# Optimization experiments

Measured on AMD Instinct MI355X. Metric: run time of the kernel, lower is better.

The kernel has to match this reference:

```python
import jax, jax.numpy as jnp
import numpy as np

VOCAB = 50257
EMB = 1024
HID = 1024
B, T = 8, 256


def setup_inputs() -> dict:
    key = jax.random.key(0)
    ks = jax.random.split(key, 6)
    s = 0.05  # small init scale for numerical sanity
    return {
        "x": jax.random.randint(ks[0], (B, T), 0, VOCAB, dtype=jnp.int64) if jax.config.jax_enable_x64 else jax.random.randint(ks[0], (B, T), 0, VOCAB, dtype=jnp.int32),
        "emb_W": jax.random.normal(ks[1], (VOCAB, EMB), dtype=jnp.float32) * s,
        "W_ih": jax.random.normal(ks[2], (4 * HID, EMB), dtype=jnp.float32) * s,
        "W_hh": jax.random.normal(ks[3], (4 * HID, HID), dtype=jnp.float32) * s,
        "b_ih": jax.random.normal(ks[4], (4 * HID,), dtype=jnp.float32) * s,
        "b_hh": jax.random.normal(ks[5], (4 * HID,), dtype=jnp.float32) * s,
        "dec_b": jnp.zeros((VOCAB,), dtype=jnp.float32),
    }


def _lstm(emb, W_ih, W_hh, b_ih, b_hh):
    # emb: [B, T, E]. Precompute input projections for all timesteps (one big GEMM).
    x_proj = jnp.einsum("bte,ge->btg", emb, W_ih) + (b_ih + b_hh)  # [B, T, 4H]
    h0 = jnp.zeros((emb.shape[0], HID), emb.dtype)
    c0 = jnp.zeros((emb.shape[0], HID), emb.dtype)

    def step(carry, xt):  # xt: [B, 4H]
        h, c = carry
        g = xt + h @ W_hh.T  # [B, 4H]
        i, f, gg, o = jnp.split(g, 4, axis=-1)  # PyTorch gate order i,f,g,o
        i = jax.nn.sigmoid(i)
        f = jax.nn.sigmoid(f)
        gg = jnp.tanh(gg)
        o = jax.nn.sigmoid(o)
        c_new = f * c + i * gg
        h_new = o * jnp.tanh(c_new)
        return (h_new, c_new), h_new

    (hT, cT), hs = jax.lax.scan(step, (h0, c0), jnp.swapaxes(x_proj, 0, 1))
    out = jnp.swapaxes(hs, 0, 1)  # [B, T, H], batch_first
    return out, (hT[None], cT[None])  # num_layers=1 leading dim


def reference(x, emb_W, W_ih, W_hh, b_ih, b_hh, dec_b):
    emb = emb_W[x]                                   # [B, T, E]
    out, hidden = _lstm(emb, W_ih, W_hh, b_ih, b_hh)  # [B, T, H]
    logits = jnp.einsum("bth,vh->btv", out, emb_W) + dec_b  # tied decoder
    logits = logits.reshape(-1, VOCAB)
    return jax.nn.log_softmax(logits, axis=1), hidden
```

## Files before the change

kernel.cpp:

```cpp
#include <hip/hip_runtime.h>

typedef float f32x4 __attribute__((ext_vector_type(4)));
typedef __bf16 bf16x8 __attribute__((ext_vector_type(8)));
typedef unsigned int u32x4 __attribute__((ext_vector_type(4)));
typedef unsigned short u16;
typedef unsigned int u32;

#define VOCAB 50257
#define KDIM 1024
#define MROWS 2048
#define TSEQ 256
#define NBLK 64
#define NHELP 192
#define NTILE 393
#define NT (NTILE * 2)
#define LOGN ((size_t)MROWS * VOCAB)

__device__ __forceinline__ u16 f2bf(float f) {
    u32 u = __builtin_bit_cast(u32, f);
    u = (u + 0x7FFFu + ((u >> 16) & 1u)) >> 16;
    return (u16)u;
}

__device__ __forceinline__ float sigm(float x) { return 1.0f / (1.0f + __expf(-x)); }

__device__ __forceinline__ u32 min4u(u32x4 v) {
    u32 a = v.x < v.y ? v.x : v.y;
    u32 b = v.z < v.w ? v.z : v.w;
    return a < b ? a : b;
}

__device__ __forceinline__ ushort4 cvt4(float4 v) {
    ushort4 o;
    o.x = f2bf(v.x); o.y = f2bf(v.y); o.z = f2bf(v.z); o.w = f2bf(v.w);
    return o;
}


__global__ __launch_bounds__(256)
void prep_all(const float4* __restrict__ Wih, ushort4* __restrict__ Wih_bf,
              const float4* __restrict__ Whh, ushort4* __restrict__ Whh_bf,
              const int* __restrict__ x, const float* __restrict__ embW,
              ushort4* __restrict__ emb_bf, u32* __restrict__ hseq,
              const float* __restrict__ bih, const float* __restrict__ bhh,
              float* __restrict__ bsum)
{
    const int bid = blockIdx.x, tid = threadIdx.x;
    if (bid < 4096) {
        long i = (long)bid * 256 + tid;
        Wih_bf[i] = cvt4(Wih[i]);
    } else if (bid < 8192) {
        long i = (long)(bid - 4096) * 256 + tid;
        Whh_bf[i] = cvt4(Whh[i]);
    } else if (bid < 10240) {
        int m = bid - 8192;
        int row = x[m];
        float4 v = ((const float4*)(embW + (size_t)row * KDIM))[tid];
        emb_bf[(size_t)m * 256 + tid] = cvt4(v);
    } else if (bid < 14352) {
        int i = (bid - 10240) * 256 + tid;
        hseq[i] = (i < 4096) ? 0x00010001u : 0u;
    } else {
        int i = (bid - 14352) * 256 + tid;
        if (i < 4096) bsum[i] = bih[i] + bhh[i];
    }
}


#define BM 128
#define BN 128
#define BK 64

__device__ __forceinline__ void gl_lds16(const u16* g, const u16* l) {
    __builtin_amdgcn_global_load_lds(
        (const __attribute__((address_space(1))) u32*)g,
        (__attribute__((address_space(3))) u32*)l, 16, 0, 0);
}

__global__ __launch_bounds__(256, 2)
void gemm_bt(const u16* __restrict__ A, const u16* __restrict__ Bm,
             const float* __restrict__ bias, float* __restrict__ C,
             int N, int Nb, int K, int ldc)
{
    __shared__ __align__(16) u16 As[BM * BK];
    __shared__ __align__(16) u16 Bs[BN * BK];
    const int tid  = threadIdx.x;
    const int lane = tid & 63;
    const int wid  = tid >> 6;

    const int gx  = gridDim.x;
    const int nwg = gx * gridDim.y;
    const int lin = blockIdx.y * gx + blockIdx.x;
    const int qq = nwg >> 3, rr = nwg & 7;
    const int xcd = lin & 7, idx = lin >> 3;
    const int neu = (xcd < rr) ? (xcd * (qq + 1) + idx)
                               : (rr * (qq + 1) + (xcd - rr) * qq + idx);
    const int bm = neu % gx;
    const int bn = neu / gx;

    const int wr = wid >> 1, wc = wid & 1;

    const u16* gA[4]; const u16* gB[4];
    const u16* ldsA[4]; const u16* ldsB[4];
#pragma unroll
    for (int r = 0; r < 4; ++r) {
        int L = r * 256 + tid;
        int row = L >> 3, ps = L & 7;
        int ls = ps ^ (row & 7);
        gA[r] = A + (size_t)(bm * BM + row) * K + ls * 8;
        int brow = bn * BN + row; brow = brow < Nb ? brow : Nb - 1;
        gB[r] = Bm + (size_t)brow * K + ls * 8;
        ldsA[r] = As + (r * 256 + wid * 64) * 8;
        ldsB[r] = Bs + (r * 256 + wid * 64) * 8;
    }

    const int lrow = lane & 15, ksl = lane >> 4;
    int aoff[4][2], boff[4][2];
#pragma unroll
    for (int i = 0; i < 4; ++i)
#pragma unroll
        for (int ks = 0; ks < 2; ++ks) {
            int ar = wr * 64 + i * 16 + lrow;
            aoff[i][ks] = ar * BK + (((ks * 4 + ksl) ^ (ar & 7)) * 8);
            int br = wc * 64 + i * 16 + lrow;
            boff[i][ks] = br * BK + (((ks * 4 + ksl) ^ (br & 7)) * 8);
        }

    f32x4 acc[4][4] = {};
    for (int kt = 0; kt < K; kt += BK) {
#pragma unroll
        for (int r = 0; r < 4; ++r) gl_lds16(gA[r] + kt, ldsA[r]);
#pragma unroll
        for (int r = 0; r < 4; ++r) gl_lds16(gB[r] + kt, ldsB[r]);
        __syncthreads();
        bf16x8 af[4][2], bfb[4][2];
#pragma unroll
        for (int i = 0; i < 4; ++i)
#pragma unroll
            for (int ks = 0; ks < 2; ++ks) {
                af[i][ks]  = *(const bf16x8*)(As + aoff[i][ks]);
                bfb[i][ks] = *(const bf16x8*)(Bs + boff[i][ks]);
            }
#pragma unroll
        for (int ks = 0; ks < 2; ++ks)
#pragma unroll
            for (int mi = 0; mi < 4; ++mi)
#pragma unroll
                for (int ni = 0; ni < 4; ++ni)
                    acc[mi][ni] = __builtin_amdgcn_mfma_f32_16x16x32_bf16(
                        af[mi][ks], bfb[ni][ks], acc[mi][ni], 0, 0, 0);
        __syncthreads();
    }

    const int crl = lane >> 4, ccl = lane & 15;
    const int row0 = bm * BM + wr * 64, col0 = bn * BN + wc * 64;
#pragma unroll
    for (int ni = 0; ni < 4; ++ni) {
        int col = col0 + ni * 16 + ccl;
        if (col < N) {
            float bv = bias[col];
#pragma unroll
            for (int mi = 0; mi < 4; ++mi) {
                int row = row0 + mi * 16 + crl * 4;
                float* cp = C + (size_t)row * ldc + col;
#pragma unroll
                for (int r = 0; r < 4; ++r)
                    cp[(size_t)r * ldc] = acc[mi][ni][r] + bv;
            }
        }
    }
}


__global__ __launch_bounds__(256, 3)
void gemm_dec(const u16* __restrict__ A, const u16* __restrict__ Bm,
              const float* __restrict__ bias, u16* __restrict__ Cb,
              float* __restrict__ pmax, float* __restrict__ psum)
{
    const int N = VOCAB, Nb = VOCAB, K = KDIM;
    __shared__ __align__(16) u16 As[BM * BK];
    __shared__ __align__(16) u16 Bs[BN * BK];
    const int tid  = threadIdx.x;
    const int lane = tid & 63;
    const int wid  = tid >> 6;

    const int gx  = gridDim.x;
    const int nwg = gx * gridDim.y;
    const int lin = blockIdx.y * gx + blockIdx.x;
    const int qq = nwg >> 3, rr = nwg & 7;
    const int xcd = lin & 7, idx = lin >> 3;
    const int neu = (xcd < rr) ? (xcd * (qq + 1) + idx)
                               : (rr * (qq + 1) + (xcd - rr) * qq + idx);
    const int bm = neu % gx;
    const int bn = neu / gx;

    const int wr = wid >> 1, wc = wid & 1;

    const u16* gA[4]; const u16* gB[4];
    const u16* ldsA[4]; const u16* ldsB[4];
#pragma unroll
    for (int r = 0; r < 4; ++r) {
        int L = r * 256 + tid;
        int row = L >> 3, ps = L & 7;
        int ls = ps ^ (row & 7);
        gA[r] = A + (size_t)(bm * BM + row) * K + ls * 8;
        int brow = bn * BN + row; brow = brow < Nb ? brow : Nb - 1;
        gB[r] = Bm + (size_t)brow * K + ls * 8;
        ldsA[r] = As + (r * 256 + wid * 64) * 8;
        ldsB[r] = Bs + (r * 256 + wid * 64) * 8;
    }

    const int lrow = lane & 15, ksl = lane >> 4;
    int aoff[4][2], boff[4][2];
#pragma unroll
    for (int i = 0; i < 4; ++i)
#pragma unroll
        for (int ks = 0; ks < 2; ++ks) {
            int ar = wr * 64 + i * 16 + lrow;
            aoff[i][ks] = ar * BK + (((ks * 4 + ksl) ^ (ar & 7)) * 8);
            int br = wc * 64 + i * 16 + lrow;
            boff[i][ks] = br * BK + (((ks * 4 + ksl) ^ (br & 7)) * 8);
        }

    f32x4 acc[4][4] = {};
    for (int kt = 0; kt < K; kt += BK) {
#pragma unroll
        for (int r = 0; r < 4; ++r) gl_lds16(gA[r] + kt, ldsA[r]);
#pragma unroll
        for (int r = 0; r < 4; ++r) gl_lds16(gB[r] + kt, ldsB[r]);
        __syncthreads();
        bf16x8 af[4][2], bfb[4][2];
#pragma unroll
        for (int i = 0; i < 4; ++i)
#pragma unroll
            for (int ks = 0; ks < 2; ++ks) {
                af[i][ks]  = *(const bf16x8*)(As + aoff[i][ks]);
                bfb[i][ks] = *(const bf16x8*)(Bs + boff[i][ks]);
            }
#pragma unroll
        for (int ks = 0; ks < 2; ++ks)
#pragma unroll
            for (int mi = 0; mi < 4; ++mi)
#pragma unroll
                for (int ni = 0; ni < 4; ++ni)
                    acc[mi][ni] = __builtin_amdgcn_mfma_f32_16x16x32_bf16(
                        af[mi][ks], bfb[ni][ks], acc[mi][ni], 0, 0, 0);
        __syncthreads();
    }

    const int crl = lane >> 4, ccl = lane & 15;
    const int row0 = bm * BM + wr * 64, col0 = bn * BN + wc * 64;
    float bve[4]; bool vld[4];
#pragma unroll
    for (int ni = 0; ni < 4; ++ni) {
        int col = col0 + ni * 16 + ccl;
        vld[ni] = col < N;
        bve[ni] = vld[ni] ? bias[col] : 0.f;
    }
#pragma unroll
    for (int ni = 0; ni < 4; ++ni) {
        if (vld[ni]) {
            int col = col0 + ni * 16 + ccl;
#pragma unroll
            for (int mi = 0; mi < 4; ++mi) {
                int row = row0 + mi * 16 + crl * 4;
                u16* cp = Cb + (size_t)row * (VOCAB * 2) + col;
#pragma unroll
                for (int r = 0; r < 4; ++r)
                    cp[(size_t)r * (VOCAB * 2)] = f2bf(acc[mi][ni][r] + bve[ni]);
            }
        }
    }
#pragma unroll
    for (int mi = 0; mi < 4; ++mi)
#pragma unroll
        for (int r = 0; r < 4; ++r) {
            int row = row0 + mi * 16 + crl * 4 + r;
            float v0 = vld[0] ? acc[mi][0][r] + bve[0] : -3.0e38f;
            float v1 = vld[1] ? acc[mi][1][r] + bve[1] : -3.0e38f;
            float v2 = vld[2] ? acc[mi][2][r] + bve[2] : -3.0e38f;
            float v3 = vld[3] ? acc[mi][3][r] + bve[3] : -3.0e38f;
            float rmax = fmaxf(fmaxf(v0, v1), fmaxf(v2, v3));
#pragma unroll
            for (int m2 = 1; m2 < 16; m2 <<= 1) rmax = fmaxf(rmax, __shfl_xor(rmax, m2));
            float rs = __expf(v0 - rmax) + __expf(v1 - rmax) +
                       __expf(v2 - rmax) + __expf(v3 - rmax);
#pragma unroll
            for (int m2 = 1; m2 < 16; m2 <<= 1) rs += __shfl_xor(rs, m2);
            if (ccl == 0) {
                pmax[(size_t)row * NT + bn * 2 + wc] = rmax;
                psum[(size_t)row * NT + bn * 2 + wc] = rs;
            }
        }
}


__global__ __launch_bounds__(256, 1)
void lstm_persist(const u16* __restrict__ Whh,
                  const float* __restrict__ xproj,
                  u16* __restrict__ hseq,
                  u16* __restrict__ hall,
                  float* __restrict__ outTail,
                  const float4* __restrict__ embW,
                  ushort4* __restrict__ embW_bf)
{
    const int tid = threadIdx.x;
    const int bid = blockIdx.x;

    if (bid >= NBLK) {
        long i = (long)(bid - NBLK) * 256 + tid;
        const long n4 = (long)VOCAB * KDIM / 4;
        const long stride = (long)NHELP * 256;
        for (; i < n4; i += stride) {
            float4 v = embW[i];
            embW_bf[i] = cvt4(v);
        }
        return;
    }

    const int lane = tid & 63;
    const int wq   = tid >> 6;
    const int lrow = lane & 15, ksl = lane >> 4;
    const int colbase = bid * 16;

    bf16x8 Bf[32];
    {
        const u16* bp = Whh + (size_t)(wq * 1024 + colbase + lrow) * KDIM + ksl * 8;
#pragma unroll
        for (int kk = 0; kk < 32; ++kk)
            asm volatile("global_load_dwordx4 %0, %1, off"
                         : "=v"(Bf[kk]) : "v"(bp + kk * 32));
        asm volatile("s_waitcnt vmcnt(0)" ::: "memory");
        __builtin_amdgcn_sched_barrier(0);
    }

    __shared__ float S[4][8][16];
    __shared__ __align__(16) u16 hstage[2][16384];

    for (int i = tid; i < 2 * 64 * 8; i += 256) {
        int buf = i >> 9, rem = i & 511;
        int j = rem >> 3, rowoff = rem & 7;
        u32x4 z = {0, 0, 0, 0};
        *(u32x4*)(&hstage[buf][j * 256 + 128 + rowoff * 16]) = z;
        *(u32x4*)(&hstage[buf][j * 256 + 128 + rowoff * 16 + 8]) = z;
    }

    const bool upd = tid < 128;
    const int b8 = tid >> 4, c16 = tid & 15;
    float creg = 0.f;
    float xp0 = 0.f, xp1 = 0.f, xp2 = 0.f, xp3 = 0.f;
    size_t xbase = 0;
    if (upd) {
        xbase = (size_t)b8 * TSEQ * 4096 + colbase + c16;
        xp0 = xproj[xbase];          xp1 = xproj[xbase + 1024];
        xp2 = xproj[xbase + 2048];   xp3 = xproj[xbase + 3072];
    }

    const int pj = tid >> 2, pr = (tid & 3) * 2;
    const int sw = (pj & 7) << 3;
    int widx[4];
#pragma unroll
    for (int k = 0; k < 4; ++k)
        widx[k] = pj * 256 + ((pr * 16 + k * 8) ^ sw);

    int aro[4];
#pragma unroll
    for (int i = 0; i < 4; ++i) {
        int swr = ((2 * i + (ksl >> 1)) & 7) << 3;
        aro[i] = (ksl >> 1) * 256 + ((lrow * 16 + (ksl & 1) * 8) ^ swr);
    }

    for (int t = 0; t < TSEQ; ++t) {
        const u32* src = (const u32*)hseq + (size_t)t * 4096 + pj * 64 + pr * 8;
        u32x4 P0, P1, P2, P3;
        for (;;) {
            asm volatile("global_load_dwordx4 %0, %1, off sc0 sc1" : "=v"(P0) : "v"(src));
            asm volatile("global_load_dwordx4 %0, %1, off sc0 sc1" : "=v"(P1) : "v"(src + 4));
            asm volatile("global_load_dwordx4 %0, %1, off sc0 sc1" : "=v"(P2) : "v"(src + 8));
            asm volatile("global_load_dwordx4 %0, %1, off sc0 sc1" : "=v"(P3) : "v"(src + 12));
            asm volatile("s_waitcnt vmcnt(0)" ::: "memory");
            __builtin_amdgcn_sched_barrier(0);
            u32 a = min4u(P0), b = min4u(P1), c = min4u(P2), d = min4u(P3);
            u32 mn = (a < b ? a : b); u32 mn2 = (c < d ? c : d);
            if ((mn < mn2 ? mn : mn2) != 0u) break;
        }
        {
            u16* hb2 = &hstage[t & 1][0];
            *(u32x4*)(hb2 + widx[0]) = P0;
            *(u32x4*)(hb2 + widx[1]) = P1;
            *(u32x4*)(hb2 + widx[2]) = P2;
            *(u32x4*)(hb2 + widx[3]) = P3;
        }
        __syncthreads();

        const u16* sb = &hstage[t & 1][0];
        f32x4 ac0 = {}, ac1 = {}, ac2 = {}, ac3 = {};
#pragma unroll
        for (int g = 0; g < 8; ++g) {
            bf16x8 a0 = *(const bf16x8*)(sb + g * 2048 + 0 * 512 + aro[0]);
            bf16x8 a1 = *(const bf16x8*)(sb + g * 2048 + 1 * 512 + aro[1]);
            bf16x8 a2 = *(const bf16x8*)(sb + g * 2048 + 2 * 512 + aro[2]);
            bf16x8 a3 = *(const bf16x8*)(sb + g * 2048 + 3 * 512 + aro[3]);
            ac0 = __builtin_amdgcn_mfma_f32_16x16x32_bf16(a0, Bf[g * 4 + 0], ac0, 0, 0, 0);
            ac1 = __builtin_amdgcn_mfma_f32_16x16x32_bf16(a1, Bf[g * 4 + 1], ac1, 0, 0, 0);
            ac2 = __builtin_amdgcn_mfma_f32_16x16x32_bf16(a2, Bf[g * 4 + 2], ac2, 0, 0, 0);
            ac3 = __builtin_amdgcn_mfma_f32_16x16x32_bf16(a3, Bf[g * 4 + 3], ac3, 0, 0, 0);
        }
        if (ksl < 2) {
#pragma unroll
            for (int r = 0; r < 4; ++r)
                S[wq][ksl * 4 + r][lrow] = ac0[r] + ac1[r] + ac2[r] + ac3[r];
        }
        __syncthreads();

        if (upd) {
            float gi = S[0][b8][c16] + xp0;
            float gf = S[1][b8][c16] + xp1;
            float gg = S[2][b8][c16] + xp2;
            float go = S[3][b8][c16] + xp3;
            float iv = sigm(gi), fv = sigm(gf), ov = sigm(go);
            float gv = tanhf(gg);
            creg = fv * creg + iv * gv;
            float hv = ov * tanhf(creg);
            u16 hbx = f2bf(hv) | 1;
            int w0 = (int)hbx;
            int w1 = __shfl_down(w0, 1);
            if (!(c16 & 1)) {
                u32 w = (u32)(u16)w0 | ((u32)(u16)w1 << 16);
                u32* dst = (u32*)hseq + (size_t)(t + 1) * 4096 + bid * 64 + b8 * 8 + (c16 >> 1);
                __hip_atomic_store(dst, w, __ATOMIC_RELAXED, __HIP_MEMORY_SCOPE_AGENT);
            }
            hall[((size_t)b8 * TSEQ + t) * KDIM + colbase + c16] = hbx;
            if (t == TSEQ - 1) {
                outTail[b8 * KDIM + colbase + c16] = hv;
                outTail[8192 + b8 * KDIM + colbase + c16] = creg;
            }
            int tn = (t + 1 < TSEQ) ? t + 1 : t;
            size_t xb = xbase + (size_t)tn * 4096;
            xp0 = xproj[xb];        xp1 = xproj[xb + 1024];
            xp2 = xproj[xb + 2048]; xp3 = xproj[xb + 3072];
        }
    }
}


__global__ __launch_bounds__(256)
void merge_final(const float* __restrict__ pmax, const float* __restrict__ psum,
                 float* __restrict__ out)
{
    const int m = blockIdx.x;
    const int tid = threadIdx.x;
    __shared__ float smx[4], ssm[4], slse;

    float mx = -3.0e38f, s = 0.f;
    for (int i = tid; i < NT; i += 256) {
        float pm = pmax[(size_t)m * NT + i];
        float ps = psum[(size_t)m * NT + i];
        if (pm > mx) { s *= __expf(mx - pm); mx = pm; }
        s += ps * __expf(pm - mx);
    }
#pragma unroll
    for (int off = 32; off > 0; off >>= 1) {
        float om = __shfl_xor(mx, off), os = __shfl_xor(s, off);
        float nm = fmaxf(mx, om);
        s = s * __expf(mx - nm) + os * __expf(om - nm);
        mx = nm;
    }
    if ((tid & 63) == 0) { smx[tid >> 6] = mx; ssm[tid >> 6] = s; }
    __syncthreads();
    if (tid == 0) {
        float M = fmaxf(fmaxf(smx[0], smx[1]), fmaxf(smx[2], smx[3]));
        float S4 = ssm[0] * __expf(smx[0] - M) + ssm[1] * __expf(smx[1] - M) +
                   ssm[2] * __expf(smx[2] - M) + ssm[3] * __expf(smx[3] - M);
        slse = M + __logf(S4);
    }
    __syncthreads();
    const float L = slse;

    const u32* srcw = (const u32*)out + (size_t)m * VOCAB;
    float* dst = out + (size_t)m * VOCAB;
    const int NCH = (VOCAB + 2047) / 2048;
    for (int c = NCH - 1; c >= 0; --c) {
        int e0 = c * 2048 + tid * 8;
        int w0i = e0 >> 1;
        u32 w0 = srcw[w0i], w1 = srcw[w0i + 1], w2 = srcw[w0i + 2], w3 = srcw[w0i + 3];
        __syncthreads();
        float f[8];
        f[0] = __builtin_bit_cast(float, (w0 & 0xFFFFu) << 16) - L;
        f[1] = __builtin_bit_cast(float, w0 & 0xFFFF0000u) - L;
        f[2] = __builtin_bit_cast(float, (w1 & 0xFFFFu) << 16) - L;
        f[3] = __builtin_bit_cast(float, w1 & 0xFFFF0000u) - L;
        f[4] = __builtin_bit_cast(float, (w2 & 0xFFFFu) << 16) - L;
        f[5] = __builtin_bit_cast(float, w2 & 0xFFFF0000u) - L;
        f[6] = __builtin_bit_cast(float, (w3 & 0xFFFFu) << 16) - L;
        f[7] = __builtin_bit_cast(float, w3 & 0xFFFF0000u) - L;
        if (e0 + 8 <= VOCAB) {
#pragma unroll
            for (int k = 0; k < 8; ++k) dst[e0 + k] = f[k];
        } else {
#pragma unroll
            for (int k = 0; k < 8; ++k) if (e0 + k < VOCAB) dst[e0 + k] = f[k];
        }
    }
}


extern "C" void kernel_launch(void* const* d_in, const int* in_sizes, int n_in,
                              void* d_out, int out_size, void* d_ws, size_t ws_size,
                              hipStream_t stream)
{
    const int*   x    = (const int*)d_in[0];
    const float* embW = (const float*)d_in[1];
    const float* Wih  = (const float*)d_in[2];
    const float* Whh  = (const float*)d_in[3];
    const float* bih  = (const float*)d_in[4];
    const float* bhh  = (const float*)d_in[5];
    const float* decb = (const float*)d_in[6];
    float* out = (float*)d_out;

    char* p = (char*)d_ws;
    auto carve = [&](size_t bytes) {
        char* q = p;
        p += (bytes + 255) & ~(size_t)255;
        return q;
    };
    u16*   embW_bf = (u16*)carve((size_t)VOCAB * KDIM * 2);
    u16*   Wih_bf  = (u16*)carve((size_t)4096 * KDIM * 2);
    u16*   Whh_bf  = (u16*)carve((size_t)4096 * KDIM * 2);
    u16*   emb_bf  = (u16*)carve((size_t)MROWS * KDIM * 2);
    float* xproj   = (float*)carve((size_t)MROWS * 4096 * 4);
    u16*   hall_bf = (u16*)carve((size_t)MROWS * KDIM * 2);
    u16*   hseq    = (u16*)carve((size_t)(TSEQ + 1) * 4096 * 4);
    float* pmax    = (float*)carve((size_t)MROWS * NT * 4);
    float* psum    = (float*)carve((size_t)MROWS * NT * 4);
    float* bsum    = (float*)carve((size_t)4096 * 4);

    prep_all<<<14368, 256, 0, stream>>>((const float4*)Wih, (ushort4*)Wih_bf,
                                        (const float4*)Whh, (ushort4*)Whh_bf,
                                        x, embW, (ushort4*)emb_bf,
                                        (u32*)hseq, bih, bhh, bsum);

    {
        dim3 g(MROWS / BM, 4096 / BN);
        gemm_bt<<<g, 256, 0, stream>>>(emb_bf, Wih_bf, bsum, xproj, 4096, 4096, KDIM, 4096);
    }

    lstm_persist<<<NBLK + NHELP, 256, 0, stream>>>(Whh_bf, xproj, hseq, hall_bf,
                                                   out + LOGN,
                                                   (const float4*)embW,
                                                   (ushort4*)embW_bf);

    {
        dim3 g(MROWS / BM, NTILE);
        gemm_dec<<<g, 256, 0, stream>>>(hall_bf, embW_bf, decb, (u16*)out, pmax, psum);
    }

    merge_final<<<MROWS, 256, 0, stream>>>(pmax, psum, out);
}
```

Before: 1.200 ms.

## Move embedding bf16 conversion from LSTM helper blocks into prep kernel

The tied-decoder weight conversion to bf16 previously ran in extra helper blocks launched alongside the persistent LSTM recurrence. It now runs as extra blocks of the prep kernel, so the LSTM launches only its 64 recurrence blocks. The aim is to stop the bandwidth-heavy conversion from contending with the latency-sensitive recurrence, at the cost of serializing the conversion before the LSTM. The per-step hidden-state store to hall is also packed into one 32-bit store per pair of lanes.

```diff
diff --git a/kernel.cpp b/kernel.cpp
--- a/kernel.cpp
+++ b/kernel.cpp
@@ -11,7 +11,6 @@
 #define MROWS 2048
 #define TSEQ 256
 #define NBLK 64
-#define NHELP 192
 #define NTILE 393
 #define NT (NTILE * 2)
 #define LOGN ((size_t)MROWS * VOCAB)
@@ -36,6 +35,13 @@
     return o;
 }
 
+
+#define PB_GATH 8192
+#define PB_HSEQ 10240
+#define PB_BIAS 14352
+#define PB_EMBW 14368
+#define PB_EMBW_N 8192
+#define PREP_BLOCKS (PB_EMBW + PB_EMBW_N)
 
 __global__ __launch_bounds__(256)
 void prep_all(const float4* __restrict__ Wih, ushort4* __restrict__ Wih_bf,
@@ -43,26 +49,32 @@
               const int* __restrict__ x, const float* __restrict__ embW,
               ushort4* __restrict__ emb_bf, u32* __restrict__ hseq,
               const float* __restrict__ bih, const float* __restrict__ bhh,
-              float* __restrict__ bsum)
+              float* __restrict__ bsum, ushort4* __restrict__ embW_bf)
 {
     const int bid = blockIdx.x, tid = threadIdx.x;
     if (bid < 4096) {
         long i = (long)bid * 256 + tid;
         Wih_bf[i] = cvt4(Wih[i]);
-    } else if (bid < 8192) {
+    } else if (bid < PB_GATH) {
         long i = (long)(bid - 4096) * 256 + tid;
         Whh_bf[i] = cvt4(Whh[i]);
-    } else if (bid < 10240) {
-        int m = bid - 8192;
+    } else if (bid < PB_HSEQ) {
+        int m = bid - PB_GATH;
         int row = x[m];
         float4 v = ((const float4*)(embW + (size_t)row * KDIM))[tid];
         emb_bf[(size_t)m * 256 + tid] = cvt4(v);
-    } else if (bid < 14352) {
-        int i = (bid - 10240) * 256 + tid;
+    } else if (bid < PB_BIAS) {
+        int i = (bid - PB_HSEQ) * 256 + tid;
         hseq[i] = (i < 4096) ? 0x00010001u : 0u;
+    } else if (bid < PB_EMBW) {
+        int i = (bid - PB_BIAS) * 256 + tid;
+        if (i < 4096) bsum[i] = bih[i] + bhh[i];
     } else {
-        int i = (bid - 14352) * 256 + tid;
-        if (i < 4096) bsum[i] = bih[i] + bhh[i];
+        long i = (long)(bid - PB_EMBW) * 256 + tid;
+        const long n4 = (long)VOCAB * KDIM / 4;
+        const long stride = (long)PB_EMBW_N * 256;
+        const float4* src = (const float4*)embW;
+        for (; i < n4; i += stride) embW_bf[i] = cvt4(src[i]);
     }
 }
 
@@ -300,23 +312,10 @@
                   const float* __restrict__ xproj,
                   u16* __restrict__ hseq,
                   u16* __restrict__ hall,
-                  float* __restrict__ outTail,
-                  const float4* __restrict__ embW,
-                  ushort4* __restrict__ embW_bf)
+                  float* __restrict__ outTail)
 {
     const int tid = threadIdx.x;
     const int bid = blockIdx.x;
-
-    if (bid >= NBLK) {
-        long i = (long)(bid - NBLK) * 256 + tid;
-        const long n4 = (long)VOCAB * KDIM / 4;
-        const long stride = (long)NHELP * 256;
-        for (; i < n4; i += stride) {
-            float4 v = embW[i];
-            embW_bf[i] = cvt4(v);
-        }
-        return;
-    }
 
     const int lane = tid & 63;
     const int wq   = tid >> 6;
@@ -426,11 +425,13 @@
             int w0 = (int)hbx;
             int w1 = __shfl_down(w0, 1);
             if (!(c16 & 1)) {
-                u32 w = (u32)(u16)w0 | ((u32)(u16)w1 << 16);
+                u32 wp = (u32)(u16)w0 | ((u32)(u16)w1 << 16);
                 u32* dst = (u32*)hseq + (size_t)(t + 1) * 4096 + bid * 64 + b8 * 8 + (c16 >> 1);
-                __hip_atomic_store(dst, w, __ATOMIC_RELAXED, __HIP_MEMORY_SCOPE_AGENT);
-            }
-            hall[((size_t)b8 * TSEQ + t) * KDIM + colbase + c16] = hbx;
+                __hip_atomic_store(dst, wp, __ATOMIC_RELAXED, __HIP_MEMORY_SCOPE_AGENT);
+                u32* hd = (u32*)hall
+                          + ((((size_t)b8 * TSEQ + t) * KDIM + colbase + c16) >> 1);
+                *hd = wp;
+            }
             if (t == TSEQ - 1) {
                 outTail[b8 * KDIM + colbase + c16] = hv;
                 outTail[8192 + b8 * KDIM + colbase + c16] = creg;
@@ -535,20 +536,18 @@
     float* psum    = (float*)carve((size_t)MROWS * NT * 4);
     float* bsum    = (float*)carve((size_t)4096 * 4);
 
-    prep_all<<<14368, 256, 0, stream>>>((const float4*)Wih, (ushort4*)Wih_bf,
-                                        (const float4*)Whh, (ushort4*)Whh_bf,
-                                        x, embW, (ushort4*)emb_bf,
-                                        (u32*)hseq, bih, bhh, bsum);
+    prep_all<<<PREP_BLOCKS, 256, 0, stream>>>((const float4*)Wih, (ushort4*)Wih_bf,
+                                              (const float4*)Whh, (ushort4*)Whh_bf,
+                                              x, embW, (ushort4*)emb_bf,
+                                              (u32*)hseq, bih, bhh, bsum,
+                                              (ushort4*)embW_bf);
 
     {
         dim3 g(MROWS / BM, 4096 / BN);
         gemm_bt<<<g, 256, 0, stream>>>(emb_bf, Wih_bf, bsum, xproj, 4096, 4096, KDIM, 4096);
     }
 
-    lstm_persist<<<NBLK + NHELP, 256, 0, stream>>>(Whh_bf, xproj, hseq, hall_bf,
-                                                   out + LOGN,
-                                                   (const float4*)embW,
-                                                   (ushort4*)embW_bf);
+    lstm_persist<<<NBLK, 256, 0, stream>>>(Whh_bf, xproj, hseq, hall_bf, out + LOGN);
 
     {
         dim3 g(MROWS / BM, NTILE);
```

Result: slower. 1.230 ms (+2.6%).
